# Kernel optimization log

Hardware: AMD Instinct MI355X
Metric: run time of the kernel (lower is better)

## Reference

```python
import jax, jax.numpy as jnp
import numpy as np

N_NODES = 100000
N_EDGES = 100000
N_MAP = 128
EPS = 1e-5


def _gn1(x, g, b):
    # GroupNorm with 1 group == per-row normalization over channels, affine per channel
    m = jnp.mean(x, axis=-1, keepdims=True)
    v = jnp.mean((x - m) ** 2, axis=-1, keepdims=True)
    return (x - m) * jax.lax.rsqrt(v + EPS) * g + b


def setup_inputs() -> dict:
    key = jax.random.key(0)
    ks = jax.random.split(key, 16)
    s = 0.02
    d = N_MAP
    inp = {
        'nodes': jax.random.normal(ks[0], (N_NODES, 8), jnp.float32),
        'indexes': jax.random.randint(ks[1], (N_EDGES, 28), 0, N_NODES, jnp.int64)
            if jax.config.jax_enable_x64 else jax.random.randint(ks[1], (N_EDGES, 28), 0, N_NODES, jnp.int32),
        'mask': jnp.full((14,), N_EDGES, dtype=jnp.int32),
        'in1_W': jax.random.normal(ks[2], (d, 2), jnp.float32) * s,
        'in1_b': jnp.zeros((d,), jnp.float32),
        'in2_W': jax.random.normal(ks[3], (d, d), jnp.float32) * s,
        'in_g': jnp.ones((d,), jnp.float32),
        'in_bg': jnp.zeros((d,), jnp.float32),
        'seg1_W': jax.random.normal(ks[4], (d, 2), jnp.float32) * s,
        'seg1_b': jnp.zeros((d,), jnp.float32),
        'seg2_W': jax.random.normal(ks[5], (d, d), jnp.float32) * s,
        'seg_g': jnp.ones((d,), jnp.float32),
        'seg_bg': jnp.zeros((d,), jnp.float32),
        'meta_W': jax.random.normal(ks[6], (d, d + 4), jnp.float32) * s,
        'meta_g': jnp.ones((d,), jnp.float32),
        'meta_bg': jnp.zeros((d,), jnp.float32),
        'ctr_W': jax.random.normal(ks[7], (4, d, d), jnp.float32) * s,
        'edge_W': jax.random.normal(ks[8], (4, 14, d, d), jnp.float32) * s,
        'norm_g': jnp.ones((4, d), jnp.float32),
        'norm_bg': jnp.zeros((4, d), jnp.float32),
        'ctr2_W': jax.random.normal(ks[9], (4, d, d), jnp.float32) * s,
        'ctr2_g': jnp.ones((4, d), jnp.float32),
        'ctr2_bg': jnp.zeros((4, d), jnp.float32),
    }
    return inp


def reference(nodes, indexes, mask, in1_W, in1_b, in2_W, in_g, in_bg,
              seg1_W, seg1_b, seg2_W, seg_g, seg_bg, meta_W, meta_g, meta_bg,
              ctr_W, edge_W, norm_g, norm_bg, ctr2_W, ctr2_g, ctr2_bg):
    relu = jax.nn.relu
    # input / seg branches: Linear+ReLU then bias-free Linear + GroupNorm(1)
    feat = _gn1(relu(nodes[:, :2] @ in1_W.T + in1_b) @ in2_W.T, in_g, in_bg)
    feat = feat + _gn1(relu(nodes[:, 2:4] @ seg1_W.T + seg1_b) @ seg2_W.T, seg_g, seg_bg)
    feat = relu(feat)
    # meta: Linear(n_map+4 -> n_map, bias-free) + GN + ReLU
    feat = relu(_gn1(jnp.concatenate([feat, nodes[:, 4:]], axis=1) @ meta_W.T, meta_g, meta_bg))
    res = feat
    E = indexes.shape[0]
    eid = jnp.arange(E)
    for i in range(4):
        temp = feat @ ctr_W[i].T
        # 14 edge types in column order: pre0..pre5, right, suc0..suc5, left
        for t in range(14):
            valid = (eid < mask[t])[:, None]          # [E,1]
            src = jnp.where(valid[:, 0], indexes[:, 2 * t + 1], 0)
            dst = jnp.where(valid[:, 0], indexes[:, 2 * t], 0)
            msg = jnp.where(valid, feat[src] @ edge_W[i, t].T, 0.0)  # [E, d]
            temp = temp.at[dst].add(msg)
        feat = relu(_gn1(temp, norm_g[i], norm_bg[i]))
        feat = _gn1(feat @ ctr2_W[i].T, ctr2_g[i], ctr2_bg[i])
        feat = relu(feat + res)
        res = feat
    return (feat, nodes[:, :2])
```

## Files before the change

kernel.cpp:

```cpp
#include <hip/hip_runtime.h>
#include <hip/hip_bf16.h>

#define NN 100000
#define NE 100000
#define NCNT (14 * NN)
#define LP 136
#define LP2 168
#define SCAN_CHUNK 4096
#define NSCB ((NCNT + SCAN_CHUNK - 1) / SCAN_CHUNK)

typedef __bf16 bf16;
typedef __bf16 bf16x8 __attribute__((ext_vector_type(8)));
typedef float  f32x4  __attribute__((ext_vector_type(4)));


__device__ __forceinline__ void gl2lds16(const bf16* g, bf16* l) {
    __builtin_amdgcn_global_load_lds(
        (const __attribute__((address_space(1))) void*)g,
        (__attribute__((address_space(3))) void*)l, 16, 0, 0);
}

__device__ __forceinline__ void zacc8(f32x4 acc[8]) {
    f32x4 z = {0.f, 0.f, 0.f, 0.f};
#pragma unroll
    for (int n = 0; n < 8; ++n) acc[n] = z;
}

__device__ __forceinline__ void gnstats(const f32x4 acc[8], float mean[4], float rs[4]) {
    float s1[4], s2[4];
#pragma unroll
    for (int r = 0; r < 4; ++r) { s1[r] = 0.f; s2[r] = 0.f; }
#pragma unroll
    for (int n = 0; n < 8; ++n)
#pragma unroll
        for (int r = 0; r < 4; ++r) { float v = acc[n][r]; s1[r] += v; s2[r] += v * v; }
#pragma unroll
    for (int off = 1; off < 16; off <<= 1) {
#pragma unroll
        for (int r = 0; r < 4; ++r) {
            s1[r] += __shfl_xor(s1[r], off, 64);
            s2[r] += __shfl_xor(s2[r], off, 64);
        }
    }
#pragma unroll
    for (int r = 0; r < 4; ++r) {
        const float m = s1[r] * 0.0078125f;
        const float v = fmaxf(s2[r] * 0.0078125f - m * m, 0.f);
        mean[r] = m;
        rs[r] = rsqrtf(v + 1e-5f);
    }
}


template<int PITCH, int COLS>
__device__ inline void stageWB(const bf16* __restrict__ Wg, bf16* Wl) {
    constexpr int NV = 128 * COLS / 8;
    for (int i = threadIdx.x; i < NV; i += 256) {
        const int e = i * 8;
        const int r = e / COLS, c = e % COLS;
        *(float4*)(&Wl[r * PITCH + c]) = ((const float4*)Wg)[i];
    }
}

template<int PITCH, int KSTEPS>
__device__ inline void mmaT(const bf16* Al, const bf16* Wl, int m0, int lane, f32x4 acc[8]) {
#pragma unroll
    for (int kk = 0; kk < KSTEPS; ++kk) {
        bf16x8 a = *(const bf16x8*)(&Al[(m0 + (lane & 15)) * PITCH + kk * 32 + (lane >> 4) * 8]);
#pragma unroll
        for (int n = 0; n < 8; ++n) {
            bf16x8 b = *(const bf16x8*)(&Wl[(n * 16 + (lane & 15)) * PITCH + kk * 32 + (lane >> 4) * 8]);
            acc[n] = __builtin_amdgcn_mfma_f32_16x16x32_bf16(a, b, acc[n], 0, 0, 0);
        }
    }
}


__device__ __forceinline__ void stageW(const bf16* __restrict__ Wg, bf16* WLbase,
                                       int w, int lane) {
#pragma unroll
    for (int k = 0; k < 4; ++k) {
        const int R = (w * 4 + k) * 4 + (lane >> 4);
        const int sg = (lane & 15) ^ ((k & 1) * 4 + (lane >> 4));
        gl2lds16(Wg + R * 128 + sg * 8, WLbase + (w * 4 + k) * 512);
    }
}

__device__ __forceinline__ void mmaW(const bf16* B, const bf16x8 afr[4],
                                     int r, int h, int r7, f32x4 acc[8]) {
#pragma unroll
    for (int kk = 0; kk < 4; ++kk) {
        const int sl = ((kk * 4 + h) ^ r7) * 8;
#pragma unroll
        for (int n = 0; n < 8; ++n) {
            const bf16x8 b = *(const bf16x8*)(B + (n * 16 + r) * 128 + sl);
            acc[n] = __builtin_amdgcn_mfma_f32_16x16x32_bf16(afr[kk], b, acc[n], 0, 0, 0);
        }
    }
}

__device__ __forceinline__ void accum_row(const bf16* __restrict__ rp, float ag[4][8]) {
    const bf16x8* q = (const bf16x8*)rp;
    bf16x8 v0 = q[0], v1 = q[4], v2 = q[8], v3 = q[12];
#pragma unroll
    for (int e = 0; e < 8; ++e) {
        ag[0][e] += (float)v0[e];
        ag[1][e] += (float)v1[e];
        ag[2][e] += (float)v2[e];
        ag[3][e] += (float)v3[e];
    }
}


__global__ void k_cvt(const float* __restrict__ s, bf16* __restrict__ d, int n) {
    for (int i = blockIdx.x * 256 + threadIdx.x; i < n; i += gridDim.x * 256)
        d[i] = (bf16)s[i];
}

__global__ void k_cvt_meta(const float* __restrict__ s, bf16* __restrict__ d) {
    for (int i = blockIdx.x * 256 + threadIdx.x; i < 128 * 160; i += gridDim.x * 256) {
        const int r = i / 160, c = i % 160;
        d[i] = (bf16)(c < 132 ? s[r * 132 + c] : 0.f);
    }
}


__global__ __launch_bounds__(256) void k_count(const int* __restrict__ idx,
                                               const int* __restrict__ mask,
                                               int* __restrict__ cnt) {
    __shared__ int lim[14];
    if (threadIdx.x < 14) lim[threadIdx.x] = min(mask[threadIdx.x], NE);
    __syncthreads();
    for (int i = blockIdx.x * 256 + threadIdx.x; i < 14 * NE; i += gridDim.x * 256) {
        const int e = i / 14, t = i - e * 14;
        if (e < lim[t]) atomicAdd(&cnt[t * NN + idx[(size_t)e * 28 + 2 * t]], 1);
    }
}

__global__ __launch_bounds__(256) void k_scanA(const int* __restrict__ cnt,
                                               int* __restrict__ ptr,
                                               int* __restrict__ tot) {
    __shared__ int sm[256];
    const int tid = threadIdx.x;
    const int base = blockIdx.x * SCAN_CHUNK + tid * 16;
    int v[16]; int run = 0;
#pragma unroll
    for (int j = 0; j < 16; ++j) {
        const int x = (base + j < NCNT) ? cnt[base + j] : 0;
        v[j] = run; run += x;
    }
    sm[tid] = run; __syncthreads();
    for (int d = 1; d < 256; d <<= 1) {
        int t = 0;
        if (tid >= d) t = sm[tid - d];
        __syncthreads();
        sm[tid] += t;
        __syncthreads();
    }
    const int off = sm[tid] - run;
#pragma unroll
    for (int j = 0; j < 16; ++j)
        if (base + j < NCNT) ptr[base + j] = v[j] + off;
    if (tid == 255) tot[blockIdx.x] = sm[255];
}

__global__ void k_scanB(int* __restrict__ tot) {
    if (threadIdx.x == 0 && blockIdx.x == 0) {
        int acc = 0;
        for (int b = 0; b < NSCB; ++b) { const int t = tot[b]; tot[b] = acc; acc += t; }
        tot[NSCB] = acc;
    }
}

__global__ __launch_bounds__(256) void k_scanC(int* __restrict__ ptr,
                                               int* __restrict__ cursor,
                                               const int* __restrict__ tot) {
    const int base = blockIdx.x * SCAN_CHUNK;
    const int o = tot[blockIdx.x];
    for (int j = threadIdx.x; j < SCAN_CHUNK; j += 256) {
        const int i = base + j;
        if (i < NCNT) { const int p = ptr[i] + o; ptr[i] = p; cursor[i] = p; }
    }
    if (blockIdx.x == 0 && threadIdx.x == 0) ptr[NCNT] = tot[NSCB];
}

__global__ __launch_bounds__(256) void k_fill(const int* __restrict__ idx,
                                              const int* __restrict__ mask,
                                              int* __restrict__ cursor,
                                              int* __restrict__ elist) {
    __shared__ int lim[14];
    if (threadIdx.x < 14) lim[threadIdx.x] = min(mask[threadIdx.x], NE);
    __syncthreads();
    for (int i = blockIdx.x * 256 + threadIdx.x; i < 14 * NE; i += gridDim.x * 256) {
        const int e = i / 14, t = i - e * 14;
        if (e < lim[t]) {
            const int dst = idx[(size_t)e * 28 + 2 * t];
            const int pos = atomicAdd(&cursor[t * NN + dst], 1);
            elist[pos] = e;
        }
    }
}

__global__ __launch_bounds__(256) void k_sortseg(const int* __restrict__ ptr,
                                                 int* __restrict__ elist,
                                                 const int* __restrict__ idx) {
    for (int i = blockIdx.x * 256 + threadIdx.x; i < NCNT; i += gridDim.x * 256) {
        const int s = ptr[i], e2 = ptr[i + 1];
        for (int a = s + 1; a < e2; ++a) {
            const int key = elist[a];
            int b = a - 1;
            while (b >= s && elist[b] > key) { elist[b + 1] = elist[b]; --b; }
            elist[b + 1] = key;
        }
        const int t = i / NN;
        for (int j = s; j < e2; ++j)
            elist[j] = idx[(size_t)elist[j] * 28 + 2 * t + 1];
    }
}


__global__ __launch_bounds__(256) void k_in(
    const float* __restrict__ nodes,
    const float* __restrict__ in1W, const float* __restrict__ in1b,
    const bf16* __restrict__ wIn2,
    const float* __restrict__ ing, const float* __restrict__ inbg,
    const float* __restrict__ seg1W, const float* __restrict__ seg1b,
    const bf16* __restrict__ wSeg2,
    const float* __restrict__ segg, const float* __restrict__ segbg,
    bf16* __restrict__ outPre)
{
    __shared__ __align__(16) bf16 Wl[128 * LP];
    __shared__ __align__(16) bf16 Al[64 * LP];
    __shared__ float w0[128], w1[128], bb[128];
    __shared__ float xs[64][4];
    const int tid = threadIdx.x;
    const int row0 = blockIdx.x * 64;
    if (tid < 64) {
        const int row = row0 + tid;
        float4 x = {0.f, 0.f, 0.f, 0.f};
        if (row < NN) x = *(const float4*)(nodes + (size_t)row * 8);
        xs[tid][0] = x.x; xs[tid][1] = x.y; xs[tid][2] = x.z; xs[tid][3] = x.w;
    }
    if (tid < 128) { w0[tid] = in1W[tid * 2]; w1[tid] = in1W[tid * 2 + 1]; bb[tid] = in1b[tid]; }
    stageWB<LP, 128>(wIn2, Wl);
    __syncthreads();
    for (int i = tid; i < 64 * 128; i += 256) {
        const int r = i >> 7, j = i & 127;
        Al[r * LP + j] = (bf16)fmaxf(xs[r][0] * w0[j] + xs[r][1] * w1[j] + bb[j], 0.f);
    }
    __syncthreads();
    const int lane = tid & 63, m0 = (tid >> 6) * 16;
    f32x4 accP[8]; zacc8(accP);
    mmaT<LP, 4>(Al, Wl, m0, lane, accP);
    __syncthreads();
    if (tid < 128) { w0[tid] = seg1W[tid * 2]; w1[tid] = seg1W[tid * 2 + 1]; bb[tid] = seg1b[tid]; }
    stageWB<LP, 128>(wSeg2, Wl);
    __syncthreads();
    for (int i = tid; i < 64 * 128; i += 256) {
        const int r = i >> 7, j = i & 127;
        Al[r * LP + j] = (bf16)fmaxf(xs[r][2] * w0[j] + xs[r][3] * w1[j] + bb[j], 0.f);
    }
    __syncthreads();
    f32x4 accQ[8]; zacc8(accQ);
    mmaT<LP, 4>(Al, Wl, m0, lane, accQ);

    float mP[4], rP[4], mQ[4], rQ[4];
    gnstats(accP, mP, rP);
    gnstats(accQ, mQ, rQ);
    float gP[8], bP[8], gQ[8], bQ[8];
#pragma unroll
    for (int n = 0; n < 8; ++n) {
        const int c = n * 16 + (lane & 15);
        gP[n] = ing[c]; bP[n] = inbg[c]; gQ[n] = segg[c]; bQ[n] = segbg[c];
    }
#pragma unroll
    for (int r = 0; r < 4; ++r) {
        const int row = row0 + m0 + (lane >> 4) * 4 + r;
        if (row < NN) {
#pragma unroll
            for (int n = 0; n < 8; ++n) {
                const float yp = (accP[n][r] - mP[r]) * rP[r] * gP[n] + bP[n];
                const float yq = (accQ[n][r] - mQ[r]) * rQ[r] * gQ[n] + bQ[n];
                outPre[(size_t)row * 128 + n * 16 + (lane & 15)] = (bf16)fmaxf(yp + yq, 0.f);
            }
        }
    }
}


__global__ __launch_bounds__(256) void k_meta(
    const bf16* __restrict__ Apre, const float* __restrict__ nodes,
    const bf16* __restrict__ Wg,
    const float* __restrict__ g, const float* __restrict__ bg,
    float* __restrict__ featF, bf16* __restrict__ featB)
{
    __shared__ __align__(16) bf16 Wl[128 * LP2];
    __shared__ __align__(16) bf16 Al[64 * LP2];
    const int row0 = blockIdx.x * 64;
    stageWB<LP2, 160>(Wg, Wl);
    {
        const int r = threadIdx.x >> 2, q = threadIdx.x & 3;
        float4* d = (float4*)(&Al[r * LP2 + q * 32]);
        const int row = row0 + r;
        if (row < NN) {
            const float4* s = (const float4*)(Apre + (size_t)row * 128 + q * 32);
            float4 a0 = s[0], a1 = s[1], a2 = s[2], a3 = s[3];
            d[0] = a0; d[1] = a1; d[2] = a2; d[3] = a3;
        } else {
            float4 z = {0.f, 0.f, 0.f, 0.f};
            d[0] = z; d[1] = z; d[2] = z; d[3] = z;
        }
    }
    if (threadIdx.x < 64) {
        const int rr = threadIdx.x, row = row0 + rr;
        bf16* d = &Al[rr * LP2 + 128];
        if (row < NN) {
            const float4 x = *(const float4*)(nodes + (size_t)row * 8 + 4);
            d[0] = (bf16)x.x; d[1] = (bf16)x.y; d[2] = (bf16)x.z; d[3] = (bf16)x.w;
        } else {
            d[0] = (bf16)0.f; d[1] = (bf16)0.f; d[2] = (bf16)0.f; d[3] = (bf16)0.f;
        }
#pragma unroll
        for (int c = 4; c < 32; ++c) d[c] = (bf16)0.f;
    }
    __syncthreads();
    const int lane = threadIdx.x & 63, m0 = (threadIdx.x >> 6) * 16;
    f32x4 acc[8]; zacc8(acc);
    mmaT<LP2, 5>(Al, Wl, m0, lane, acc);

    float mean[4], rs[4];
    gnstats(acc, mean, rs);
    float gv[8], bv[8];
#pragma unroll
    for (int n = 0; n < 8; ++n) { const int c = n * 16 + (lane & 15); gv[n] = g[c]; bv[n] = bg[c]; }
#pragma unroll
    for (int r = 0; r < 4; ++r) {
        const int row = row0 + m0 + (lane >> 4) * 4 + r;
        if (row < NN) {
            const size_t off = (size_t)row * 128 + (lane & 15);
#pragma unroll
            for (int n = 0; n < 8; ++n) {
                const float y = (acc[n][r] - mean[r]) * rs[r] * gv[n] + bv[n];
                const float o = fmaxf(y, 0.f);
                featF[off + n * 16] = o;
                featB[off + n * 16] = (bf16)o;
            }
        }
    }
}


__global__ __launch_bounds__(512, 4) void k_round(
    const bf16* __restrict__ feat,
    const int* __restrict__ ptr,
    const int* __restrict__ slist,
    const bf16* __restrict__ wEdgeR,
    const bf16* __restrict__ wCtrR,
    const bf16* __restrict__ wCtr2R,
    const float* __restrict__ ng, const float* __restrict__ nbg,
    const float* __restrict__ c2g, const float* __restrict__ c2bg,
    float* __restrict__ featF,
    bf16* __restrict__ featOut,
    float* __restrict__ outF,
    int last)
{
    __shared__ __align__(16) bf16 WL[2 * 16384];
    const int tid = threadIdx.x;
    const int w = tid >> 6, lane = tid & 63;
    const int r = lane & 15, h = lane >> 4, r7 = r & 7;
    const int m0 = w * 16;
    const int row0 = blockIdx.x * 128;
    const int grow = row0 + m0 + r;
    const bool rowok = grow < NN;

    stageW(wEdgeR, WL, w, lane);

    int p0 = 0, p1 = 0;
    if (rowok) { p0 = ptr[grow]; p1 = ptr[grow + 1]; }
    int sA = slist[p1 > p0 ? p0 : 0];

    f32x4 acc[8]; zacc8(acc);

    for (int t = 0; t < 15; ++t) {
        float ag[4][8];
#pragma unroll
        for (int kk = 0; kk < 4; ++kk)
#pragma unroll
            for (int e = 0; e < 8; ++e) ag[kk][e] = 0.f;

        if (t < 14) {
            if (rowok && p1 > p0) {
                accum_row(feat + (size_t)sA * 128 + h * 8, ag);
                for (int j = p0 + 1; j < p1; ++j)
                    accum_row(feat + (size_t)slist[j] * 128 + h * 8, ag);
            }
        } else if (rowok) {
            accum_row(feat + (size_t)grow * 128 + h * 8, ag);
        }

        if (t < 13) {
            int q0 = 0, q1 = 0;
            if (rowok) {
                const size_t i2 = (size_t)(t + 1) * NN + grow;
                q0 = ptr[i2]; q1 = ptr[i2 + 1];
            }
            const int sN = slist[q1 > q0 ? q0 : 0];
            p0 = q0; p1 = q1; sA = sN;
        }

        bf16x8 afr[4];
#pragma unroll
        for (int kk = 0; kk < 4; ++kk)
#pragma unroll
            for (int e = 0; e < 8; ++e) afr[kk][e] = (bf16)ag[kk][e];

        asm volatile("s_waitcnt vmcnt(0)" ::: "memory");
        __builtin_amdgcn_s_barrier();
        __builtin_amdgcn_sched_barrier(0);
        if (t < 13)       stageW(wEdgeR + (size_t)(t + 1) * 16384, WL + ((t + 1) & 1) * 16384, w, lane);
        else if (t == 13) stageW(wCtrR,  WL,          w, lane);
        else              stageW(wCtr2R, WL + 16384,  w, lane);
        __builtin_amdgcn_sched_barrier(0);
        mmaW(WL + (t & 1) * 16384, afr, r, h, r7, acc);
    }

    float mean[4], rsv[4];
    gnstats(acc, mean, rsv);
    float gv[8], bv[8];
#pragma unroll
    for (int n = 0; n < 8; ++n) { const int c = n * 16 + r; gv[n] = ng[c]; bv[n] = nbg[c]; }
    asm volatile("s_waitcnt vmcnt(0)" ::: "memory");
    __builtin_amdgcn_s_barrier();
    __builtin_amdgcn_sched_barrier(0);
#pragma unroll
    for (int r2 = 0; r2 < 4; ++r2) {
        const int lrow = m0 + h * 4 + r2;
#pragma unroll
        for (int n = 0; n < 8; ++n) {
            const float y = (acc[n][r2] - mean[r2]) * rsv[r2] * gv[n] + bv[n];
            const int col = n * 16 + r;
            const int slot = (col >> 3) ^ (lrow & 7);
            *(bf16*)((char*)WL + lrow * 256 + slot * 16 + (col & 7) * 2) = (bf16)fmaxf(y, 0.f);
        }
    }
    asm volatile("s_waitcnt lgkmcnt(0)" ::: "memory");
    __builtin_amdgcn_s_barrier();
    __builtin_amdgcn_sched_barrier(0);

    bf16x8 afr2[4];
    {
        const int arow = m0 + r;
#pragma unroll
        for (int kk = 0; kk < 4; ++kk) {
            const int slot = (kk * 4 + h) ^ (arow & 7);
            afr2[kk] = *(const bf16x8*)((const char*)WL + arow * 256 + slot * 16);
        }
    }
    zacc8(acc);
    mmaW(WL + 16384, afr2, r, h, r7, acc);

    gnstats(acc, mean, rsv);
#pragma unroll
    for (int n = 0; n < 8; ++n) { const int c = n * 16 + r; gv[n] = c2g[c]; bv[n] = c2bg[c]; }
#pragma unroll
    for (int r2 = 0; r2 < 4; ++r2) {
        const int orow = row0 + m0 + h * 4 + r2;
        if (orow < NN) {
            const size_t off = (size_t)orow * 128 + r;
#pragma unroll
            for (int n = 0; n < 8; ++n) {
                const float y = (acc[n][r2] - mean[r2]) * rsv[r2] * gv[n] + bv[n];
                const float o = fmaxf(y + featF[off + n * 16], 0.f);
                if (last) {
                    outF[off + n * 16] = o;
                } else {
                    featF[off + n * 16] = o;
                    featOut[off + n * 16] = (bf16)o;
                }
            }
        }
    }
}


__global__ void k_nodes(const float* __restrict__ nodes, float* __restrict__ out) {
    const int j = blockIdx.x * 256 + threadIdx.x;
    if (j < 2 * NN) out[(size_t)NN * 128 + j] = nodes[(size_t)(j >> 1) * 8 + (j & 1)];
}


extern "C" void kernel_launch(void* const* d_in, const int* in_sizes, int n_in,
                              void* d_out, int out_size, void* d_ws, size_t ws_size,
                              hipStream_t stream) {
    const float* nodes  = (const float*)d_in[0];
    const int*   idx    = (const int*)d_in[1];
    const int*   mask   = (const int*)d_in[2];
    const float* in1W   = (const float*)d_in[3];
    const float* in1b   = (const float*)d_in[4];
    const float* in2W   = (const float*)d_in[5];
    const float* ing    = (const float*)d_in[6];
    const float* inbg   = (const float*)d_in[7];
    const float* seg1W  = (const float*)d_in[8];
    const float* seg1b  = (const float*)d_in[9];
    const float* seg2W  = (const float*)d_in[10];
    const float* segg   = (const float*)d_in[11];
    const float* segbg  = (const float*)d_in[12];
    const float* metaW  = (const float*)d_in[13];
    const float* metag  = (const float*)d_in[14];
    const float* metabg = (const float*)d_in[15];
    const float* ctrW   = (const float*)d_in[16];
    const float* edgeW  = (const float*)d_in[17];
    const float* normg  = (const float*)d_in[18];
    const float* normbg = (const float*)d_in[19];
    const float* ctr2W  = (const float*)d_in[20];
    const float* ctr2g  = (const float*)d_in[21];
    const float* ctr2bg = (const float*)d_in[22];
    float* out = (float*)d_out;

    char* w = (char*)d_ws;
    float* featF  = (float*)w; w += (size_t)NN * 128 * 4;
    bf16*  featB0 = (bf16*)w;  w += (size_t)NN * 128 * 2;
    bf16*  featB1 = (bf16*)w;  w += (size_t)NN * 128 * 2;
    bf16*  preB   = (bf16*)w;  w += (size_t)NN * 128 * 2;
    bf16*  wIn2   = (bf16*)w;  w += 16384 * 2;
    bf16*  wSeg2  = (bf16*)w;  w += 16384 * 2;
    bf16*  wMeta  = (bf16*)w;  w += 20480 * 2;
    bf16*  wCtr   = (bf16*)w;  w += 65536 * 2;
    bf16*  wCtr2  = (bf16*)w;  w += 65536 * 2;
    bf16*  wEdge  = (bf16*)w;  w += (size_t)917504 * 2;
    int*   cnt    = (int*)w;   w += (size_t)NCNT * 4;
    int*   ptr    = (int*)w;   w += ((size_t)NCNT + 4) * 4;
    int*   cursor = (int*)w;   w += (size_t)NCNT * 4;
    int*   elist  = (int*)w;   w += (size_t)14 * NE * 4;
    int*   tot    = (int*)w;   w += (NSCB + 1) * 4;

    dim3 blk(256);
    const int gRows = (NN + 63) / 64;

    hipMemsetAsync(cnt, 0, (size_t)NCNT * 4, stream);
    k_count<<<2048, blk, 0, stream>>>(idx, mask, cnt);
    k_scanA<<<NSCB, blk, 0, stream>>>(cnt, ptr, tot);
    k_scanB<<<1, 64, 0, stream>>>(tot);
    k_scanC<<<NSCB, blk, 0, stream>>>(ptr, cursor, tot);
    k_fill<<<2048, blk, 0, stream>>>(idx, mask, cursor, elist);
    k_sortseg<<<2048, blk, 0, stream>>>(ptr, elist, idx);

    k_cvt<<<64, blk, 0, stream>>>(in2W, wIn2, 16384);
    k_cvt<<<64, blk, 0, stream>>>(seg2W, wSeg2, 16384);
    k_cvt_meta<<<80, blk, 0, stream>>>(metaW, wMeta);
    k_cvt<<<256, blk, 0, stream>>>(ctrW, wCtr, 65536);
    k_cvt<<<256, blk, 0, stream>>>(ctr2W, wCtr2, 65536);
    k_cvt<<<2048, blk, 0, stream>>>(edgeW, wEdge, 917504);

    k_in<<<gRows, blk, 0, stream>>>(nodes, in1W, in1b, wIn2, ing, inbg,
                                    seg1W, seg1b, wSeg2, segg, segbg, preB);
    k_meta<<<gRows, blk, 0, stream>>>(preB, nodes, wMeta, metag, metabg, featF, featB0);

    bf16* bufs[2] = { featB0, featB1 };
    const int gR2 = (NN + 127) / 128;
    for (int i = 0; i < 4; ++i) {
        k_round<<<gR2, dim3(512), 0, stream>>>(bufs[i & 1], ptr, elist,
                                               wEdge + (size_t)i * 14 * 16384,
                                               wCtr + (size_t)i * 16384,
                                               wCtr2 + (size_t)i * 16384,
                                               normg + i * 128, normbg + i * 128,
                                               ctr2g + i * 128, ctr2bg + i * 128,
                                               featF, bufs[(i + 1) & 1], out,
                                               i == 3 ? 1 : 0);
    }
    k_nodes<<<(2 * NN + 255) / 256, blk, 0, stream>>>(nodes, out);
}
```

Before: 1.074 ms.

## Process two row tiles per wave and pack edge-src pairs into 64-bit list

k_round now runs 256 threads per block, with each wave handling 32 rows as two 16-row MFMA tiles. Each LDS B-fragment read is shared across two MFMAs, and each wave stages twice as many weight rows. The gather loop prefetches the first two source indices and the next type's pointers two steps ahead, so more loads are in flight. The edge list stores (edge id, src) as a u64, which lets the sort key on edge order and drops the post-sort idx lookup. The cost is higher register pressure (two accumulator sets, occupancy hint 2) and doubled edge-list memory.

```diff
diff --git a/kernel.cpp b/kernel.cpp
--- a/kernel.cpp
+++ b/kernel.cpp
@@ -12,6 +12,7 @@
 typedef __bf16 bf16;
 typedef __bf16 bf16x8 __attribute__((ext_vector_type(8)));
 typedef float  f32x4  __attribute__((ext_vector_type(4)));
+typedef unsigned long long u64;
 
 
 __device__ __forceinline__ void gl2lds16(const bf16* g, bf16* l) {
@@ -79,36 +80,38 @@
 __device__ __forceinline__ void stageW(const bf16* __restrict__ Wg, bf16* WLbase,
                                        int w, int lane) {
 #pragma unroll
-    for (int k = 0; k < 4; ++k) {
-        const int R = (w * 4 + k) * 4 + (lane >> 4);
+    for (int k = 0; k < 8; ++k) {
+        const int R = (w * 8 + k) * 4 + (lane >> 4);
         const int sg = (lane & 15) ^ ((k & 1) * 4 + (lane >> 4));
-        gl2lds16(Wg + R * 128 + sg * 8, WLbase + (w * 4 + k) * 512);
-    }
-}
-
-__device__ __forceinline__ void mmaW(const bf16* B, const bf16x8 afr[4],
-                                     int r, int h, int r7, f32x4 acc[8]) {
+        gl2lds16(Wg + R * 128 + sg * 8, WLbase + (w * 8 + k) * 512);
+    }
+}
+
+__device__ __forceinline__ void mmaW2(const bf16* B, const bf16x8 aA[4], const bf16x8 aB[4],
+                                      int r, int h, int r7, f32x4 accA[8], f32x4 accB[8]) {
 #pragma unroll
     for (int kk = 0; kk < 4; ++kk) {
         const int sl = ((kk * 4 + h) ^ r7) * 8;
 #pragma unroll
         for (int n = 0; n < 8; ++n) {
             const bf16x8 b = *(const bf16x8*)(B + (n * 16 + r) * 128 + sl);
-            acc[n] = __builtin_amdgcn_mfma_f32_16x16x32_bf16(afr[kk], b, acc[n], 0, 0, 0);
-        }
-    }
-}
-
-__device__ __forceinline__ void accum_row(const bf16* __restrict__ rp, float ag[4][8]) {
-    const bf16x8* q = (const bf16x8*)rp;
-    bf16x8 v0 = q[0], v1 = q[4], v2 = q[8], v3 = q[12];
-#pragma unroll
-    for (int e = 0; e < 8; ++e) {
-        ag[0][e] += (float)v0[e];
-        ag[1][e] += (float)v1[e];
-        ag[2][e] += (float)v2[e];
-        ag[3][e] += (float)v3[e];
-    }
+            accA[n] = __builtin_amdgcn_mfma_f32_16x16x32_bf16(aA[kk], b, accA[n], 0, 0, 0);
+            accB[n] = __builtin_amdgcn_mfma_f32_16x16x32_bf16(aB[kk], b, accB[n], 0, 0, 0);
+        }
+    }
+}
+
+__device__ __forceinline__ void loadrow(bf16x8 e[4], const bf16* __restrict__ feat,
+                                        int s, int h) {
+    const bf16x8* q = (const bf16x8*)(feat + (size_t)s * 128 + h * 8);
+    e[0] = q[0]; e[1] = q[4]; e[2] = q[8]; e[3] = q[12];
+}
+
+__device__ __forceinline__ void faccum(float ag[4][8], const bf16x8 e[4]) {
+#pragma unroll
+    for (int kk = 0; kk < 4; ++kk)
+#pragma unroll
+        for (int j = 0; j < 8; ++j) ag[kk][j] += (float)e[kk][j];
 }
 
 
@@ -187,7 +190,7 @@
 __global__ __launch_bounds__(256) void k_fill(const int* __restrict__ idx,
                                               const int* __restrict__ mask,
                                               int* __restrict__ cursor,
-                                              int* __restrict__ elist) {
+                                              u64* __restrict__ el) {
     __shared__ int lim[14];
     if (threadIdx.x < 14) lim[threadIdx.x] = min(mask[threadIdx.x], NE);
     __syncthreads();
@@ -195,26 +198,23 @@
         const int e = i / 14, t = i - e * 14;
         if (e < lim[t]) {
             const int dst = idx[(size_t)e * 28 + 2 * t];
+            const int src = idx[(size_t)e * 28 + 2 * t + 1];
             const int pos = atomicAdd(&cursor[t * NN + dst], 1);
-            elist[pos] = e;
+            el[pos] = ((u64)(unsigned)e << 32) | (unsigned)src;
         }
     }
 }
 
 __global__ __launch_bounds__(256) void k_sortseg(const int* __restrict__ ptr,
-                                                 int* __restrict__ elist,
-                                                 const int* __restrict__ idx) {
+                                                 u64* __restrict__ el) {
     for (int i = blockIdx.x * 256 + threadIdx.x; i < NCNT; i += gridDim.x * 256) {
         const int s = ptr[i], e2 = ptr[i + 1];
         for (int a = s + 1; a < e2; ++a) {
-            const int key = elist[a];
+            const u64 key = el[a];
             int b = a - 1;
-            while (b >= s && elist[b] > key) { elist[b + 1] = elist[b]; --b; }
-            elist[b + 1] = key;
-        }
-        const int t = i / NN;
-        for (int j = s; j < e2; ++j)
-            elist[j] = idx[(size_t)elist[j] * 28 + 2 * t + 1];
+            while (b >= s && el[b] > key) { el[b + 1] = el[b]; --b; }
+            el[b + 1] = key;
+        }
     }
 }
 
@@ -350,10 +350,10 @@
 }
 
 
-__global__ __launch_bounds__(512, 4) void k_round(
+__global__ __launch_bounds__(256, 2) void k_round(
     const bf16* __restrict__ feat,
     const int* __restrict__ ptr,
-    const int* __restrict__ slist,
+    const int* __restrict__ sl32,
     const bf16* __restrict__ wEdgeR,
     const bf16* __restrict__ wCtrR,
     const bf16* __restrict__ wCtr2R,
@@ -368,51 +368,95 @@
     const int tid = threadIdx.x;
     const int w = tid >> 6, lane = tid & 63;
     const int r = lane & 15, h = lane >> 4, r7 = r & 7;
-    const int m0 = w * 16;
     const int row0 = blockIdx.x * 128;
-    const int grow = row0 + m0 + r;
-    const bool rowok = grow < NN;
+    const int gA = row0 + w * 32 + r;
+    const int gB = gA + 16;
+    const bool okA = gA < NN, okB = gB < NN;
 
     stageW(wEdgeR, WL, w, lane);
 
-    int p0 = 0, p1 = 0;
-    if (rowok) { p0 = ptr[grow]; p1 = ptr[grow + 1]; }
-    int sA = slist[p1 > p0 ? p0 : 0];
-
-    f32x4 acc[8]; zacc8(acc);
+    int pA0 = 0, pA1 = 0, pB0 = 0, pB1 = 0;
+    if (okA) { pA0 = ptr[gA]; pA1 = ptr[gA + 1]; }
+    if (okB) { pB0 = ptr[gB]; pB1 = ptr[gB + 1]; }
+    int sA0 = 0, sA1 = 0, sB0 = 0, sB1 = 0;
+    if (pA1 > pA0)     sA0 = sl32[2 * pA0];
+    if (pA1 > pA0 + 1) sA1 = sl32[2 * (pA0 + 1)];
+    if (pB1 > pB0)     sB0 = sl32[2 * pB0];
+    if (pB1 > pB0 + 1) sB1 = sl32[2 * (pB0 + 1)];
+    int nA0 = 0, nA1 = 0, nB0 = 0, nB1 = 0;
+    if (okA) { nA0 = ptr[NN + gA]; nA1 = ptr[NN + gA + 1]; }
+    if (okB) { nB0 = ptr[NN + gB]; nB1 = ptr[NN + gB + 1]; }
+
+    f32x4 accA[8], accB[8];
+    zacc8(accA); zacc8(accB);
 
     for (int t = 0; t < 15; ++t) {
-        float ag[4][8];
-#pragma unroll
-        for (int kk = 0; kk < 4; ++kk)
-#pragma unroll
-            for (int e = 0; e < 8; ++e) ag[kk][e] = 0.f;
-
+        bf16x8 afrA[4], afrB[4];
         if (t < 14) {
-            if (rowok && p1 > p0) {
-                accum_row(feat + (size_t)sA * 128 + h * 8, ag);
-                for (int j = p0 + 1; j < p1; ++j)
-                    accum_row(feat + (size_t)slist[j] * 128 + h * 8, ag);
+            bf16x8 eA0[4], eA1[4], eB0[4], eB1[4];
+            const int dA = pA1 - pA0, dB = pB1 - pB0;
+            if (dA > 0) loadrow(eA0, feat, sA0, h);
+            if (dA > 1) loadrow(eA1, feat, sA1, h);
+            if (dB > 0) loadrow(eB0, feat, sB0, h);
+            if (dB > 1) loadrow(eB1, feat, sB1, h);
+            int tsA0 = 0, tsA1 = 0, tsB0 = 0, tsB1 = 0;
+            if (t < 13) {
+                if (nA1 > nA0)     tsA0 = sl32[2 * nA0];
+                if (nA1 > nA0 + 1) tsA1 = sl32[2 * (nA0 + 1)];
+                if (nB1 > nB0)     tsB0 = sl32[2 * nB0];
+                if (nB1 > nB0 + 1) tsB1 = sl32[2 * (nB0 + 1)];
             }
-        } else if (rowok) {
-            accum_row(feat + (size_t)grow * 128 + h * 8, ag);
-        }
-
-        if (t < 13) {
-            int q0 = 0, q1 = 0;
-            if (rowok) {
-                const size_t i2 = (size_t)(t + 1) * NN + grow;
-                q0 = ptr[i2]; q1 = ptr[i2 + 1];
+            int mA0 = 0, mA1 = 0, mB0 = 0, mB1 = 0;
+            if (t < 12) {
+                const size_t b2 = (size_t)(t + 2) * NN;
+                if (okA) { mA0 = ptr[b2 + gA]; mA1 = ptr[b2 + gA + 1]; }
+                if (okB) { mB0 = ptr[b2 + gB]; mB1 = ptr[b2 + gB + 1]; }
             }
-            const int sN = slist[q1 > q0 ? q0 : 0];
-            p0 = q0; p1 = q1; sA = sN;
-        }
-
-        bf16x8 afr[4];
-#pragma unroll
-        for (int kk = 0; kk < 4; ++kk)
-#pragma unroll
-            for (int e = 0; e < 8; ++e) afr[kk][e] = (bf16)ag[kk][e];
+            float ag[4][8];
+#pragma unroll
+            for (int kk = 0; kk < 4; ++kk)
+#pragma unroll
+                for (int j = 0; j < 8; ++j) ag[kk][j] = 0.f;
+            if (dA > 0) faccum(ag, eA0);
+            if (dA > 1) faccum(ag, eA1);
+            for (int j = pA0 + 2; j < pA1; ++j) {
+                bf16x8 e[4];
+                loadrow(e, feat, sl32[2 * j], h);
+                faccum(ag, e);
+            }
+#pragma unroll
+            for (int kk = 0; kk < 4; ++kk)
+#pragma unroll
+                for (int j = 0; j < 8; ++j) afrA[kk][j] = (bf16)ag[kk][j];
+#pragma unroll
+            for (int kk = 0; kk < 4; ++kk)
+#pragma unroll
+                for (int j = 0; j < 8; ++j) ag[kk][j] = 0.f;
+            if (dB > 0) faccum(ag, eB0);
+            if (dB > 1) faccum(ag, eB1);
+            for (int j = pB0 + 2; j < pB1; ++j) {
+                bf16x8 e[4];
+                loadrow(e, feat, sl32[2 * j], h);
+                faccum(ag, e);
+            }
+#pragma unroll
+            for (int kk = 0; kk < 4; ++kk)
+#pragma unroll
+                for (int j = 0; j < 8; ++j) afrB[kk][j] = (bf16)ag[kk][j];
+            pA0 = nA0; pA1 = nA1; pB0 = nB0; pB1 = nB1;
+            sA0 = tsA0; sA1 = tsA1; sB0 = tsB0; sB1 = tsB1;
+            nA0 = mA0; nA1 = mA1; nB0 = mB0; nB1 = mB1;
+        } else {
+            bf16x8 e[4];
+            if (okA) { loadrow(e, feat, gA, h); } else { e[0]=e[1]=e[2]=e[3]=bf16x8{}; }
+#pragma unroll
+            for (int kk = 0; kk < 4; ++kk) afrA[kk] = e[kk];
+            if (okB) { loadrow(e, feat, gB, h); } else { e[0]=e[1]=e[2]=e[3]=bf16x8{}; }
+#pragma unroll
+            for (int kk = 0; kk < 4; ++kk) afrB[kk] = e[kk];
+        }
+        if (!okA) { bf16x8 z{}; afrA[0]=afrA[1]=afrA[2]=afrA[3]=z; }
+        if (!okB) { bf16x8 z{}; afrB[0]=afrB[1]=afrB[2]=afrB[3]=z; }
 
         asm volatile("s_waitcnt vmcnt(0)" ::: "memory");
         __builtin_amdgcn_s_barrier();
@@ -421,11 +465,12 @@
         else if (t == 13) stageW(wCtrR,  WL,          w, lane);
         else              stageW(wCtr2R, WL + 16384,  w, lane);
         __builtin_amdgcn_sched_barrier(0);
-        mmaW(WL + (t & 1) * 16384, afr, r, h, r7, acc);
-    }
-
-    float mean[4], rsv[4];
-    gnstats(acc, mean, rsv);
+        mmaW2(WL + (t & 1) * 16384, afrA, afrB, r, h, r7, accA, accB);
+    }
+
+    float meanA[4], rsA[4], meanB[4], rsB[4];
+    gnstats(accA, meanA, rsA);
+    gnstats(accB, meanB, rsB);
     float gv[8], bv[8];
 #pragma unroll
     for (int n = 0; n < 8; ++n) { const int c = n * 16 + r; gv[n] = ng[c]; bv[n] = nbg[c]; }
@@ -434,48 +479,61 @@
     __builtin_amdgcn_sched_barrier(0);
 #pragma unroll
     for (int r2 = 0; r2 < 4; ++r2) {
-        const int lrow = m0 + h * 4 + r2;
+        const int lrowA = w * 32 + h * 4 + r2;
+        const int lrowB = lrowA + 16;
 #pragma unroll
         for (int n = 0; n < 8; ++n) {
-            const float y = (acc[n][r2] - mean[r2]) * rsv[r2] * gv[n] + bv[n];
             const int col = n * 16 + r;
-            const int slot = (col >> 3) ^ (lrow & 7);
-            *(bf16*)((char*)WL + lrow * 256 + slot * 16 + (col & 7) * 2) = (bf16)fmaxf(y, 0.f);
+            const float yA = (accA[n][r2] - meanA[r2]) * rsA[r2] * gv[n] + bv[n];
+            const float yB = (accB[n][r2] - meanB[r2]) * rsB[r2] * gv[n] + bv[n];
+            const int slA = (col >> 3) ^ (lrowA & 7);
+            const int slB = (col >> 3) ^ (lrowB & 7);
+            *(bf16*)((char*)WL + lrowA * 256 + slA * 16 + (col & 7) * 2) = (bf16)fmaxf(yA, 0.f);
+            *(bf16*)((char*)WL + lrowB * 256 + slB * 16 + (col & 7) * 2) = (bf16)fmaxf(yB, 0.f);
         }
     }
     asm volatile("s_waitcnt lgkmcnt(0)" ::: "memory");
     __builtin_amdgcn_s_barrier();
     __builtin_amdgcn_sched_barrier(0);
 
-    bf16x8 afr2[4];
+    bf16x8 afrA2[4], afrB2[4];
     {
-        const int arow = m0 + r;
+        const int arowA = w * 32 + r, arowB = arowA + 16;
 #pragma unroll
         for (int kk = 0; kk < 4; ++kk) {
-            const int slot = (kk * 4 + h) ^ (arow & 7);
-            afr2[kk] = *(const bf16x8*)((const char*)WL + arow * 256 + slot * 16);
-        }
-    }
-    zacc8(acc);
-    mmaW(WL + 16384, afr2, r, h, r7, acc);
-
-    gnstats(acc, mean, rsv);
+            const int slA = (kk * 4 + h) ^ (arowA & 7);
+            const int slB = (kk * 4 + h) ^ (arowB & 7);
+            afrA2[kk] = *(const bf16x8*)((const char*)WL + arowA * 256 + slA * 16);
+            afrB2[kk] = *(const bf16x8*)((const char*)WL + arowB * 256 + slB * 16);
+        }
+    }
+    zacc8(accA); zacc8(accB);
+    mmaW2(WL + 16384, afrA2, afrB2, r, h, r7, accA, accB);
+
+    gnstats(accA, meanA, rsA);
+    gnstats(accB, meanB, rsB);
 #pragma unroll
     for (int n = 0; n < 8; ++n) { const int c = n * 16 + r; gv[n] = c2g[c]; bv[n] = c2bg[c]; }
 #pragma unroll
-    for (int r2 = 0; r2 < 4; ++r2) {
-        const int orow = row0 + m0 + h * 4 + r2;
-        if (orow < NN) {
-            const size_t off = (size_t)orow * 128 + r;
-#pragma unroll
-            for (int n = 0; n < 8; ++n) {
-                const float y = (acc[n][r2] - mean[r2]) * rsv[r2] * gv[n] + bv[n];
-                const float o = fmaxf(y + featF[off + n * 16], 0.f);
-                if (last) {
-                    outF[off + n * 16] = o;
-                } else {
-                    featF[off + n * 16] = o;
-                    featOut[off + n * 16] = (bf16)o;
+    for (int mi = 0; mi < 2; ++mi) {
+        const f32x4* acc = mi ? accB : accA;
+        const float* mean = mi ? meanB : meanA;
+        const float* rsv = mi ? rsB : rsA;
+#pragma unroll
+        for (int r2 = 0; r2 < 4; ++r2) {
+            const int orow = row0 + w * 32 + mi * 16 + h * 4 + r2;
+            if (orow < NN) {
+                const size_t off = (size_t)orow * 128 + r;
+#pragma unroll
+                for (int n = 0; n < 8; ++n) {
+                    const float y = (acc[n][r2] - mean[r2]) * rsv[r2] * gv[n] + bv[n];
+                    const float o = fmaxf(y + featF[off + n * 16], 0.f);
+                    if (last) {
+                        outF[off + n * 16] = o;
+                    } else {
+                        featF[off + n * 16] = o;
+                        featOut[off + n * 16] = (bf16)o;
+                    }
                 }
             }
         }
@@ -531,7 +589,7 @@
     int*   cnt    = (int*)w;   w += (size_t)NCNT * 4;
     int*   ptr    = (int*)w;   w += ((size_t)NCNT + 4) * 4;
     int*   cursor = (int*)w;   w += (size_t)NCNT * 4;
-    int*   elist  = (int*)w;   w += (size_t)14 * NE * 4;
+    u64*   elist  = (u64*)w;   w += (size_t)14 * NE * 8 + 64;
     int*   tot    = (int*)w;   w += (NSCB + 1) * 4;
 
     dim3 blk(256);
@@ -543,7 +601,7 @@
     k_scanB<<<1, 64, 0, stream>>>(tot);
     k_scanC<<<NSCB, blk, 0, stream>>>(ptr, cursor, tot);
     k_fill<<<2048, blk, 0, stream>>>(idx, mask, cursor, elist);
-    k_sortseg<<<2048, blk, 0, stream>>>(ptr, elist, idx);
+    k_sortseg<<<2048, blk, 0, stream>>>(ptr, elist);
 
     k_cvt<<<64, blk, 0, stream>>>(in2W, wIn2, 16384);
     k_cvt<<<64, blk, 0, stream>>>(seg2W, wSeg2, 16384);
@@ -559,14 +617,14 @@
     bf16* bufs[2] = { featB0, featB1 };
     const int gR2 = (NN + 127) / 128;
     for (int i = 0; i < 4; ++i) {
-        k_round<<<gR2, dim3(512), 0, stream>>>(bufs[i & 1], ptr, elist,
-                                               wEdge + (size_t)i * 14 * 16384,
-                                               wCtr + (size_t)i * 16384,
-                                               wCtr2 + (size_t)i * 16384,
-                                               normg + i * 128, normbg + i * 128,
-                                               ctr2g + i * 128, ctr2bg + i * 128,
-                                               featF, bufs[(i + 1) & 1], out,
-                                               i == 3 ? 1 : 0);
+        k_round<<<gR2, blk, 0, stream>>>(bufs[i & 1], ptr, (const int*)elist,
+                                         wEdge + (size_t)i * 14 * 16384,
+                                         wCtr + (size_t)i * 16384,
+                                         wCtr2 + (size_t)i * 16384,
+                                         normg + i * 128, normbg + i * 128,
+                                         ctr2g + i * 128, ctr2bg + i * 128,
+                                         featF, bufs[(i + 1) & 1], out,
+                                         i == 3 ? 1 : 0);
     }
     k_nodes<<<(2 * NN + 255) / 256, blk, 0, stream>>>(nodes, out);
 }
```

New measurement: 2.105 ms. +96.0%, slower.
